# Optimization experiments

Measured on AMD Instinct MI355X. Metric: run time of the kernel, lower is better.

Reference implementation:

```python
import jax, jax.numpy as jnp
import numpy as np

B, L, W, M, NL = 8, 2048, 32, 16, 4  # batch, seq len, width, modes, num_layers


def setup_inputs() -> dict:
    key = jax.random.key(0)
    ks = jax.random.split(key, 16)
    u = lambda k, s: jax.random.uniform(k, s, dtype=jnp.float32)
    n = lambda k, s, sc=0.05: jax.random.normal(k, s, dtype=jnp.float32) * sc
    return {
        "x": jax.random.normal(ks[0], (B, L, 1), dtype=jnp.float32),
        "t": jnp.linspace(0.0, 1.0, L, dtype=jnp.float32),  # grid_x_train
        "fc0_w": n(ks[1], (W, 2), 0.5), "fc0_b": n(ks[2], (W,), 0.1),
        # PR params (torch.rand cfloat -> uniform[0,1) real & imag)
        "pole_re": u(ks[3], (NL, W, W, M)), "pole_im": u(ks[4], (NL, W, W, M)),
        "res_re": u(ks[5], (NL, W, W, M)), "res_im": u(ks[6], (NL, W, W, M)),
        # SpectralConv1d params
        "spec_re": u(ks[7], (NL, W, W, M)), "spec_im": u(ks[8], (NL, W, W, M)),
        # 1x1 Conv1d params
        "conv_w": n(ks[9], (NL, W, W)), "conv_b": n(ks[10], (NL, W), 0.01),
        "fc1_w": n(ks[11], (128, W)), "fc1_b": n(ks[12], (128,), 0.01),
        "fc2_w": n(ks[13], (1, 128)), "fc2_b": n(ks[14], (1,), 0.01),
    }


def reference(x, t, fc0_w, fc0_b, pole_re, pole_im, res_re, res_im,
              spec_re, spec_im, conv_w, conv_b, fc1_w, fc1_b, fc2_w, fc2_b):
    Bx, Lx, _ = x.shape
    gelu = lambda v: jax.nn.gelu(v, approximate=False)
    # get_grid + fc0 + gelu, then (B, L, W) -> (B, W, L)
    grid = jnp.broadcast_to(jnp.linspace(0.0, 1.0, Lx, dtype=x.dtype)[None, :, None], (Bx, Lx, 1))
    h = gelu(jnp.concatenate([x, grid], axis=-1) @ fc0_w.T + fc0_b)
    h = jnp.transpose(h, (0, 2, 1))  # (B, W, L)

    dt = t[1] - t[0]
    # lambda = fftfreq(L, dt) * 2*pi*1j (purely imaginary)
    freqs = jnp.fft.fftfreq(Lx).astype(x.dtype) / dt * (2.0 * np.pi)  # (L,)
    lam = jax.lax.complex(jnp.zeros_like(freqs), freqs)  # complex64 (L,)

    for i in range(NL):
        # --- PR (pole-residue Laplace) branch ---
        pole = jax.lax.complex(pole_re[i], pole_im[i])  # (in, out, M)
        res = jax.lax.complex(res_re[i], res_im[i])     # (in, out, M)
        alpha = jnp.fft.fft(h, axis=-1)  # (B, in, L) complex
        # broadcast-reduce: (in, out, L, M) -> sum over modes -> (in, out, L)
        Hw = (res[:, :, None, :] / (lam[None, None, :, None] - pole[:, :, None, :])).sum(-1)
        pr = jnp.real(jnp.fft.ifft(jnp.einsum('bix,iox->box', alpha, Hw), n=Lx, axis=-1))
        # --- SpectralConv1d branch ---
        spec_w = jax.lax.complex(spec_re[i], spec_im[i])  # (in, out, M)
        xf = jnp.fft.rfft(h, axis=-1)  # (B, in, L//2+1)
        out_ft = jnp.zeros_like(xf).at[:, :, :M].set(
            jnp.einsum('bix,iox->box', xf[:, :, :M], spec_w))
        sc = jnp.fft.irfft(out_ft, n=Lx, axis=-1)
        # --- 1x1 conv branch ---
        wv = jnp.einsum('bil,oi->bol', h, conv_w[i]) + conv_b[i][None, :, None]
        h = gelu(pr + sc + wv)

    h = jnp.transpose(h, (0, 2, 1))  # (B, L, W)
    h = gelu(h @ fc1_w.T + fc1_b)
    return h @ fc2_w.T + fc2_b  # (B, L, 1)
```

## Files before the change

### kernel.cpp

```cpp
#include <hip/hip_runtime.h>
#include <math.h>

#define NFFT   2048
#define M2     1024
#define LOG2N  11
#define BB     8
#define WW     32
#define MM     16
#define NLAYER 4
#define AST    1032

#define PAD(i) ((i) + ((i) >> 5))
#define PADDED_M (M2 + (M2 >> 5))

__device__ __forceinline__ float gelu_f(float v) {
    float ax = fabsf(v) * 0.70710678118654752440f;
    float t  = __builtin_amdgcn_rcpf(fmaf(0.3275911f, ax, 1.0f));
    float s  = fmaf(1.061405429f, t, -1.453152027f);
    s = fmaf(s, t, 1.421413741f);
    s = fmaf(s, t, -0.284496736f);
    s = fmaf(s, t, 0.254829592f);
    s = s * t;
    float e  = __expf(-ax * ax);
    float er = fmaf(-s, e, 1.0f);
    er = copysignf(er, v);
    return 0.5f * v * (1.0f + er);
}

__device__ __forceinline__ float2 cadd(float2 a, float2 b) { return make_float2(a.x + b.x, a.y + b.y); }
__device__ __forceinline__ float2 csub(float2 a, float2 b) { return make_float2(a.x - b.x, a.y - b.y); }
__device__ __forceinline__ float2 cmul(float2 a, float2 b) {
    return make_float2(fmaf(a.x, b.x, -a.y * b.y), fmaf(a.x, b.y, a.y * b.x));
}
template<int S> __device__ __forceinline__ float2 caddi(float2 a, float2 b) {
    return (S > 0) ? make_float2(a.x - b.y, a.y + b.x) : make_float2(a.x + b.y, a.y - b.x);
}
template<int S> __device__ __forceinline__ float2 csubi(float2 a, float2 b) {
    return (S > 0) ? make_float2(a.x + b.y, a.y - b.x) : make_float2(a.x - b.y, a.y + b.x);
}

template<int S> __device__ __forceinline__ void dft4(float2* a) {
    float2 t0 = cadd(a[0], a[2]), t1 = csub(a[0], a[2]);
    float2 t2 = cadd(a[1], a[3]), t3 = csub(a[1], a[3]);
    a[0] = cadd(t0, t2);
    a[2] = csub(t0, t2);
    a[1] = caddi<S>(t1, t3);
    a[3] = csubi<S>(t1, t3);
}

template<int LS, int S>
__device__ __forceinline__ void pass_r4(const float* sre, const float* sim,
                                        float* dre, float* dim, int t) {
    const int s = t & (LS - 1);
    const int q = t / LS;
    float2 a[4];
    #pragma unroll
    for (int r = 0; r < 4; ++r) {
        int idx = t + r * 256;
        a[r] = make_float2(sre[PAD(idx)], sim[PAD(idx)]);
    }
    if (LS > 1) {
        float ph = (6.2831853071795864769f / (4.0f * (float)LS)) * (float)s;
        float sn, cs;
        __sincosf(ph, &sn, &cs);
        float2 w1 = make_float2(cs, (S > 0) ? sn : -sn);
        float2 w2 = cmul(w1, w1);
        a[1] = cmul(a[1], w1);
        a[2] = cmul(a[2], w2);
        a[3] = cmul(a[3], cmul(w2, w1));
    }
    dft4<S>(a);
    int base = q * (4 * LS) + s;
    #pragma unroll
    for (int r = 0; r < 4; ++r) {
        int idx = base + r * LS;
        dre[PAD(idx)] = a[r].x;
        dim[PAD(idx)] = a[r].y;
    }
}

template<int S>
__device__ __forceinline__ void fft1024_g(float* Ar, float* Ai, float* Br, float* Bi,
                                          int t, bool act) {
    if (act) pass_r4<1,   S>(Ar, Ai, Br, Bi, t);
    __syncthreads();
    if (act) pass_r4<4,   S>(Br, Bi, Ar, Ai, t);
    __syncthreads();
    if (act) pass_r4<16,  S>(Ar, Ai, Br, Bi, t);
    __syncthreads();
    if (act) pass_r4<64,  S>(Br, Bi, Ar, Ai, t);
    __syncthreads();
    if (act) pass_r4<256, S>(Ar, Ai, Br, Bi, t);
    __syncthreads();
}

__global__ __launch_bounds__(256) void k_genG_fc0(
    const float* __restrict__ pole_re, const float* __restrict__ pole_im,
    const float* __restrict__ res_re,  const float* __restrict__ res_im,
    const float* __restrict__ spec_re, const float* __restrict__ spec_im,
    const float* __restrict__ conv_w,  const float* __restrict__ tgrid,
    const float* __restrict__ x,       const float* __restrict__ fc0_w,
    const float* __restrict__ fc0_b,
    float2* __restrict__ G, float2* __restrict__ alpha)
{
    __shared__ float Ar[PADDED_M], Ai[PADDED_M], Br[PADDED_M], Bi[PADDED_M];
    int t = threadIdx.x;
    int blk = blockIdx.x;
    float dt = tgrid[1] - tgrid[0];
    float fscale = 6.2831853071795864769f / ((float)NFFT * dt);

    if (blk < NLAYER * WW * WW) {
        int l = blk >> 10, r = blk & 1023, o = r >> 5, i = r & 31;
        int pb = ((l * WW + i) * WW + o) * MM;
        float cw = conv_w[(l * WW + o) * WW + i];
        float wv[4], w2[4];
        float2 acc[4];
        #pragma unroll
        for (int kk = 0; kk < 4; ++kk) {
            wv[kk] = fscale * (float)(t + kk * 256);
            w2[kk] = wv[kk] * wv[kk];
            acc[kk] = make_float2(cw, 0.0f);
        }
        #pragma unroll
        for (int mq = 0; mq < 4; ++mq) {
            float4 P_re = *(const float4*)&pole_re[pb + 4 * mq];
            float4 P_im = *(const float4*)&pole_im[pb + 4 * mq];
            float4 R_re = *(const float4*)&res_re [pb + 4 * mq];
            float4 R_im = *(const float4*)&res_im [pb + 4 * mq];
            #pragma unroll
            for (int mm = 0; mm < 4; ++mm) {
                float Rp = (&P_re.x)[mm], Ip = (&P_im.x)[mm];
                float Rr = (&R_re.x)[mm], Ir = (&R_im.x)[mm];
                float b   = fmaf(Rr, Rp, Ir * Ip);
                float c   = fmaf(Rp, Rp, Ip * Ip);
                float dd  = 2.0f * Rp;
                float dd2 = dd * dd;
                float add = Rr * dd;
                float bdd = b * dd;
                #pragma unroll
                for (int kk = 0; kk < 4; ++kk) {
                    float u   = c - w2[kk];
                    float inv = __builtin_amdgcn_rcpf(fmaf(dd2, w2[kk], u * u));
                    acc[kk].x = fmaf(fmaf(add, w2[kk], b * u), -inv, acc[kk].x);
                    acc[kk].y = fmaf(fmaf(Rr, u, -bdd) * inv, wv[kk], acc[kk].y);
                }
            }
        }
        if (t < MM) {
            if (t) {
                acc[0].x += spec_re[pb + t];
                acc[0].y += spec_im[pb + t];
            } else {
                acc[0].x += spec_re[pb];
            }
        }
        float2* grow = G + (size_t)((l * WW + o) * WW + i) * AST;
        #pragma unroll
        for (int kk = 0; kk < 4; ++kk) grow[t + kk * 256] = acc[kk];
        if (t < 64) {
            float wn = -fscale * (float)M2;
            float accn = cw;
            #pragma unroll
            for (int mq = 0; mq < 4; ++mq) {
                float4 P_re = *(const float4*)&pole_re[pb + 4 * mq];
                float4 P_im = *(const float4*)&pole_im[pb + 4 * mq];
                float4 R_re = *(const float4*)&res_re [pb + 4 * mq];
                float4 R_im = *(const float4*)&res_im [pb + 4 * mq];
                #pragma unroll
                for (int mm = 0; mm < 4; ++mm) {
                    float Rp = (&P_re.x)[mm], Ip = (&P_im.x)[mm];
                    float Rr = (&R_re.x)[mm], Ir = (&R_im.x)[mm];
                    float e   = wn - Ip;
                    float num = fmaf(Ir, e, -(Rr * Rp));
                    float den = fmaf(e, e, Rp * Rp);
                    accn += num * __builtin_amdgcn_rcpf(den);
                }
            }
            if (t == 0) grow[M2] = make_float2(accn, 0.0f);
        }
    } else {
        int row = blk - NLAYER * WW * WW;
        int b = row >> 5, w = row & 31;
        float w0 = fc0_w[2 * w], w1 = fc0_w[2 * w + 1], b0 = fc0_b[w];
        #pragma unroll
        for (int j = 0; j < 8; ++j) {
            int idx = t + j * 256;
            float xv = x[b * NFFT + idx];
            float gv = (float)idx * (1.0f / 2047.0f);
            float val = gelu_f(fmaf(w0, xv, fmaf(w1, gv, b0)));
            int n = idx >> 1;
            if (idx & 1) Ai[PAD(n)] = val;
            else         Ar[PAD(n)] = val;
        }
        __syncthreads();
        fft1024_g<-1>(Ar, Ai, Br, Bi, t, true);
        #pragma unroll
        for (int j = 0; j < 4; ++j) {
            int k  = t + j * 256;
            int mk = (M2 - k) & (M2 - 1);
            float2 Zk  = make_float2(Br[PAD(k)],  Bi[PAD(k)]);
            float2 Zmk = make_float2(Br[PAD(mk)], Bi[PAD(mk)]);
            float2 A  = make_float2(0.5f * (Zk.x + Zmk.x), 0.5f * (Zk.y - Zmk.y));
            float2 Bv = make_float2(0.5f * (Zk.y + Zmk.y), -0.5f * (Zk.x - Zmk.x));
            float ph = (3.1415926535897932385f / (float)M2) * (float)k;
            float sn, cs;
            __sincosf(ph, &sn, &cs);
            float2 e = make_float2(cs, -sn);
            float2 X = cadd(A, cmul(Bv, e));
            float2* arow = alpha + (size_t)row * AST;
            arow[k] = X;
            if (k == 0) arow[M2] = make_float2(A.x - Bv.x, 0.0f);
        }
    }
}

__device__ __forceinline__ void unpack_store512(const float* Br, const float* Bi,
                                                float2* __restrict__ arow, int t) {
    #pragma unroll
    for (int j = 0; j < 2; ++j) {
        int k  = t + j * 512;
        int mk = (M2 - k) & (M2 - 1);
        float2 Zk  = make_float2(Br[PAD(k)],  Bi[PAD(k)]);
        float2 Zmk = make_float2(Br[PAD(mk)], Bi[PAD(mk)]);
        float2 A  = make_float2(0.5f * (Zk.x + Zmk.x), 0.5f * (Zk.y - Zmk.y));
        float2 Bv = make_float2(0.5f * (Zk.y + Zmk.y), -0.5f * (Zk.x - Zmk.x));
        float ph = (3.1415926535897932385f / (float)M2) * (float)k;
        float sn, cs;
        __sincosf(ph, &sn, &cs);
        float2 e = make_float2(cs, -sn);
        float2 X = cadd(A, cmul(Bv, e));
        arow[k] = X;
        if (k == 0)
            arow[M2] = make_float2(A.x - Bv.x, 0.0f);
    }
}

template<bool LAST>
__global__ __launch_bounds__(512) void k_apply_fft(
    const float2* __restrict__ alpha, const float2* __restrict__ G,
    const float* __restrict__ conv_b, float2* __restrict__ alpha_next,
    float2* __restrict__ hout, int layer)
{
    __shared__ float Yr[M2 + 2], Yi[M2 + 2];
    __shared__ float Ar[PADDED_M], Ai[PADDED_M], Br[PADDED_M], Bi[PADDED_M];
    int t = threadIdx.x;
    int row = blockIdx.x;
    int b = row >> 5, o = row & 31;
    const float2* abase = alpha + (size_t)(b * WW) * AST;
    const float2* gbase = G + (size_t)((layer * WW + o) * WW) * AST;

    float2 acc0 = make_float2(0.0f, 0.0f);
    float2 acc1 = make_float2(0.0f, 0.0f);
    #pragma unroll 4
    for (int i = 0; i < 32; ++i) {
        float2 a0 = abase[(size_t)i * AST + t];
        float2 g0 = gbase[(size_t)i * AST + t];
        float2 a1 = abase[(size_t)i * AST + t + 512];
        float2 g1 = gbase[(size_t)i * AST + t + 512];
        acc0.x = fmaf(a0.x, g0.x, fmaf(-a0.y, g0.y, acc0.x));
        acc0.y = fmaf(a0.x, g0.y, fmaf( a0.y, g0.x, acc0.y));
        acc1.x = fmaf(a1.x, g1.x, fmaf(-a1.y, g1.y, acc1.x));
        acc1.y = fmaf(a1.x, g1.y, fmaf( a1.y, g1.x, acc1.y));
    }
    if (t < 64) {
        float p = 0.0f;
        if (t < 32)
            p = abase[(size_t)t * AST + M2].x * gbase[(size_t)t * AST + M2].x;
        #pragma unroll
        for (int off = 16; off >= 1; off >>= 1) p += __shfl_xor(p, off);
        if (t == 0) { Yr[M2] = p; Yi[M2] = 0.0f; }
    }
    if (t == 0) acc0.x += (float)NFFT * conv_b[layer * WW + o];
    Yr[t] = acc0.x;        Yi[t] = acc0.y;
    Yr[t + 512] = acc1.x;  Yi[t + 512] = acc1.y;
    __syncthreads();

    #pragma unroll
    for (int j = 0; j < 2; ++j) {
        int k = t + j * 512;
        float2 Xk = make_float2(Yr[k], Yi[k]);
        float2 Xm = make_float2(Yr[M2 - k], Yi[M2 - k]);
        float2 A = make_float2(0.5f * (Xk.x + Xm.x), 0.5f * (Xk.y - Xm.y));
        float2 u = make_float2(Xk.x - Xm.x, Xk.y + Xm.y);
        float ph = (3.1415926535897932385f / (float)M2) * (float)k;
        float sn, cs;
        __sincosf(ph, &sn, &cs);
        float2 e = make_float2(cs, sn);
        float2 Bv = cmul(u, e);
        Ar[PAD(k)] = A.x - 0.5f * Bv.y;
        Ai[PAD(k)] = A.y + 0.5f * Bv.x;
    }
    __syncthreads();
    fft1024_g<1>(Ar, Ai, Br, Bi, t, t < 256);
    const float invM = 1.0f / (float)M2;
    if (LAST) {
        #pragma unroll
        for (int j = 0; j < 2; ++j) {
            int n = t + j * 512;
            float ge = gelu_f(Br[PAD(n)] * invM);
            float go = gelu_f(Bi[PAD(n)] * invM);
            hout[(size_t)row * M2 + n] = make_float2(ge, go);
        }
    } else {
        #pragma unroll
        for (int j = 0; j < 2; ++j) {
            int n = t + j * 512;
            float ge = gelu_f(Br[PAD(n)] * invM);
            float go = gelu_f(Bi[PAD(n)] * invM);
            Ar[PAD(n)] = ge;
            Ai[PAD(n)] = go;
        }
        __syncthreads();
        fft1024_g<-1>(Ar, Ai, Br, Bi, t, t < 256);
        unpack_store512(Br, Bi, alpha_next + (size_t)row * AST, t);
    }
}

__global__ __launch_bounds__(256) void k_head(
    const float* __restrict__ h, const float* __restrict__ fc1_w,
    const float* __restrict__ fc1_b, const float* __restrict__ fc2_w,
    const float* __restrict__ fc2_b, float* __restrict__ out)
{
    __shared__ float s_w1[128 * 32];
    __shared__ float s_b1[128];
    __shared__ float s_w2[128];
    __shared__ float s_part[4][64];
    int t = threadIdx.x;
    for (int j = t; j < 128 * 32; j += 256) s_w1[j] = fc1_w[j];
    if (t < 128) { s_b1[t] = fc1_b[t]; s_w2[t] = fc2_w[t]; }
    __syncthreads();
    int wv  = t >> 6;
    int ln  = t & 63;
    int pos = blockIdx.x * 64 + ln;
    int b = pos >> LOG2N, l = pos & (NFFT - 1);
    float hreg[32];
    #pragma unroll
    for (int w = 0; w < 32; ++w) hreg[w] = h[(b * WW + w) * NFFT + l];
    float acc = 0.0f;
    int n0 = wv * 32;
    for (int n = n0; n < n0 + 32; ++n) {
        float a = s_b1[n];
        #pragma unroll
        for (int w = 0; w < 32; w += 4) {
            float4 ww = *(const float4*)&s_w1[n * 32 + w];
            a = fmaf(ww.x, hreg[w],     a);
            a = fmaf(ww.y, hreg[w + 1], a);
            a = fmaf(ww.z, hreg[w + 2], a);
            a = fmaf(ww.w, hreg[w + 3], a);
        }
        acc = fmaf(s_w2[n], gelu_f(a), acc);
    }
    s_part[wv][ln] = acc;
    __syncthreads();
    if (t < 64) {
        float r = s_part[0][t] + s_part[1][t] + s_part[2][t] + s_part[3][t] + fc2_b[0];
        out[blockIdx.x * 64 + t] = r;
    }
}

extern "C" void kernel_launch(void* const* d_in, const int* in_sizes, int n_in,
                              void* d_out, int out_size, void* d_ws, size_t ws_size,
                              hipStream_t stream)
{
    const float* x       = (const float*)d_in[0];
    const float* tg      = (const float*)d_in[1];
    const float* fc0_w   = (const float*)d_in[2];
    const float* fc0_b   = (const float*)d_in[3];
    const float* pole_re = (const float*)d_in[4];
    const float* pole_im = (const float*)d_in[5];
    const float* res_re  = (const float*)d_in[6];
    const float* res_im  = (const float*)d_in[7];
    const float* spec_re = (const float*)d_in[8];
    const float* spec_im = (const float*)d_in[9];
    const float* conv_w  = (const float*)d_in[10];
    const float* conv_b  = (const float*)d_in[11];
    const float* fc1_w   = (const float*)d_in[12];
    const float* fc1_b   = (const float*)d_in[13];
    const float* fc2_w   = (const float*)d_in[14];
    const float* fc2_b   = (const float*)d_in[15];
    float* out = (float*)d_out;

    char* ws = (char*)d_ws;
    const size_t plane = (size_t)(BB * WW) * AST * sizeof(float2);
    float2* alphaA = (float2*)ws;
    float2* alphaB = (float2*)(ws + plane);
    float2* hbuf   = (float2*)(ws + 2 * plane);
    float2* Gbuf   = (float2*)(ws + 3 * plane + (size_t)(BB * WW) * M2 * sizeof(float2));

    hipLaunchKernelGGL(k_genG_fc0, dim3(NLAYER * WW * WW + BB * WW), dim3(256), 0, stream,
                       pole_re, pole_im, res_re, res_im, spec_re, spec_im,
                       conv_w, tg, x, fc0_w, fc0_b, Gbuf, alphaA);
    float2* acur = alphaA;
    float2* anxt = alphaB;
    for (int layer = 0; layer < NLAYER; ++layer) {
        if (layer < NLAYER - 1)
            hipLaunchKernelGGL((k_apply_fft<false>), dim3(BB * WW), dim3(512), 0, stream,
                               acur, Gbuf, conv_b, anxt, (float2*)nullptr, layer);
        else
            hipLaunchKernelGGL((k_apply_fft<true>), dim3(BB * WW), dim3(512), 0, stream,
                               acur, Gbuf, conv_b, (float2*)nullptr, hbuf, layer);
        float2* tmp = acur; acur = anxt; anxt = tmp;
    }
    hipLaunchKernelGGL(k_head, dim3(BB * NFFT / 64), dim3(256), 0, stream,
                       (const float*)hbuf, fc1_w, fc1_b, fc2_w, fc2_b, out);
}
```

Baseline: 103.9 us.

## Interleave FFT shared buffers, precompute twiddles, and remap G generation to wavefronts

FFT scratch moves from split real/imag float arrays to interleaved float2 arrays, and each thread computes its per-stage twiddles once with make_tw instead of calling sincos in every radix-4 pass. G generation now assigns one 64-lane wavefront per (layer,o,i) row with 16 frequencies per lane, so four rows share a block and the grid shrinks, and the multiply by wv is hoisted out of the mode loop. The alpha·G contraction loads float4 pairs of adjacent frequencies, and the fc0 input is read as float2. The cost is more registers in the G kernel (16 complex accumulators per lane), which may lower occupancy.

```diff
diff --git a/kernel.cpp b/kernel.cpp
--- a/kernel.cpp
+++ b/kernel.cpp
@@ -49,48 +49,48 @@
 }
 
 template<int LS, int S>
-__device__ __forceinline__ void pass_r4(const float* sre, const float* sim,
-                                        float* dre, float* dim, int t) {
-    const int s = t & (LS - 1);
-    const int q = t / LS;
+__device__ __forceinline__ void pass_cx(const float2* src, float2* dst, int t, float2 w1f) {
     float2 a[4];
     #pragma unroll
-    for (int r = 0; r < 4; ++r) {
-        int idx = t + r * 256;
-        a[r] = make_float2(sre[PAD(idx)], sim[PAD(idx)]);
-    }
+    for (int r = 0; r < 4; ++r) a[r] = src[PAD(t + r * 256)];
     if (LS > 1) {
-        float ph = (6.2831853071795864769f / (4.0f * (float)LS)) * (float)s;
-        float sn, cs;
-        __sincosf(ph, &sn, &cs);
-        float2 w1 = make_float2(cs, (S > 0) ? sn : -sn);
+        float2 w1 = (S > 0) ? make_float2(w1f.x, -w1f.y) : w1f;
         float2 w2 = cmul(w1, w1);
+        float2 w3 = cmul(w2, w1);
         a[1] = cmul(a[1], w1);
         a[2] = cmul(a[2], w2);
-        a[3] = cmul(a[3], cmul(w2, w1));
+        a[3] = cmul(a[3], w3);
     }
     dft4<S>(a);
-    int base = q * (4 * LS) + s;
+    int s = t & (LS - 1);
+    int base = (t / LS) * (4 * LS) + s;
     #pragma unroll
-    for (int r = 0; r < 4; ++r) {
-        int idx = base + r * LS;
-        dre[PAD(idx)] = a[r].x;
-        dim[PAD(idx)] = a[r].y;
-    }
+    for (int r = 0; r < 4; ++r) dst[PAD(base + r * LS)] = a[r];
+}
+
+struct Tw { float2 t4, t16, t64, t256; };
+__device__ __forceinline__ Tw make_tw(int t) {
+    Tw w;
+    float sn, cs;
+    const float c0 = 6.2831853071795864769f;
+    __sincosf(c0 * (float)(t & 3)   * (1.0f / 16.0f),   &sn, &cs); w.t4   = make_float2(cs, -sn);
+    __sincosf(c0 * (float)(t & 15)  * (1.0f / 64.0f),   &sn, &cs); w.t16  = make_float2(cs, -sn);
+    __sincosf(c0 * (float)(t & 63)  * (1.0f / 256.0f),  &sn, &cs); w.t64  = make_float2(cs, -sn);
+    __sincosf(c0 * (float)(t & 255) * (1.0f / 1024.0f), &sn, &cs); w.t256 = make_float2(cs, -sn);
+    return w;
 }
 
 template<int S>
-__device__ __forceinline__ void fft1024_g(float* Ar, float* Ai, float* Br, float* Bi,
-                                          int t, bool act) {
-    if (act) pass_r4<1,   S>(Ar, Ai, Br, Bi, t);
-    __syncthreads();
-    if (act) pass_r4<4,   S>(Br, Bi, Ar, Ai, t);
-    __syncthreads();
-    if (act) pass_r4<16,  S>(Ar, Ai, Br, Bi, t);
-    __syncthreads();
-    if (act) pass_r4<64,  S>(Br, Bi, Ar, Ai, t);
-    __syncthreads();
-    if (act) pass_r4<256, S>(Ar, Ai, Br, Bi, t);
+__device__ __forceinline__ void fft1024_cx(float2* A, float2* B, int t, bool act, const Tw& w) {
+    if (act) pass_cx<1,   S>(A, B, t, make_float2(1.0f, 0.0f));
+    __syncthreads();
+    if (act) pass_cx<4,   S>(B, A, t, w.t4);
+    __syncthreads();
+    if (act) pass_cx<16,  S>(A, B, t, w.t16);
+    __syncthreads();
+    if (act) pass_cx<64,  S>(B, A, t, w.t64);
+    __syncthreads();
+    if (act) pass_cx<256, S>(A, B, t, w.t256);
     __syncthreads();
 }
 
@@ -103,23 +103,25 @@
     const float* __restrict__ fc0_b,
     float2* __restrict__ G, float2* __restrict__ alpha)
 {
-    __shared__ float Ar[PADDED_M], Ai[PADDED_M], Br[PADDED_M], Bi[PADDED_M];
+    __shared__ float2 Acx[PADDED_M], Bcx[PADDED_M];
     int t = threadIdx.x;
     int blk = blockIdx.x;
     float dt = tgrid[1] - tgrid[0];
     float fscale = 6.2831853071795864769f / ((float)NFFT * dt);
 
-    if (blk < NLAYER * WW * WW) {
-        int l = blk >> 10, r = blk & 1023, o = r >> 5, i = r & 31;
+    if (blk < NLAYER * WW * WW / 4) {
+        int lane = t & 63;
+        int u = blk * 4 + (t >> 6);
+        int l = u >> 10, r = u & 1023, o = r >> 5, i = r & 31;
         int pb = ((l * WW + i) * WW + o) * MM;
         float cw = conv_w[(l * WW + o) * WW + i];
-        float wv[4], w2[4];
-        float2 acc[4];
-        #pragma unroll
-        for (int kk = 0; kk < 4; ++kk) {
-            wv[kk] = fscale * (float)(t + kk * 256);
-            w2[kk] = wv[kk] * wv[kk];
-            acc[kk] = make_float2(cw, 0.0f);
+        float w2r[16];
+        float2 acc[16];
+        #pragma unroll
+        for (int j = 0; j < 16; ++j) {
+            float wv = fscale * (float)(lane + 64 * j);
+            w2r[j] = wv * wv;
+            acc[j] = make_float2(cw, 0.0f);
         }
         #pragma unroll
         for (int mq = 0; mq < 4; ++mq) {
@@ -138,26 +140,29 @@
                 float add = Rr * dd;
                 float bdd = b * dd;
                 #pragma unroll
-                for (int kk = 0; kk < 4; ++kk) {
-                    float u   = c - w2[kk];
-                    float inv = __builtin_amdgcn_rcpf(fmaf(dd2, w2[kk], u * u));
-                    acc[kk].x = fmaf(fmaf(add, w2[kk], b * u), -inv, acc[kk].x);
-                    acc[kk].y = fmaf(fmaf(Rr, u, -bdd) * inv, wv[kk], acc[kk].y);
+                for (int j = 0; j < 16; ++j) {
+                    float uu  = c - w2r[j];
+                    float inv = __builtin_amdgcn_rcpf(fmaf(dd2, w2r[j], uu * uu));
+                    acc[j].x = fmaf(fmaf(add, w2r[j], b * uu), -inv, acc[j].x);
+                    acc[j].y = fmaf(fmaf(Rr, uu, -bdd), inv, acc[j].y);
                 }
             }
         }
-        if (t < MM) {
-            if (t) {
-                acc[0].x += spec_re[pb + t];
-                acc[0].y += spec_im[pb + t];
+        #pragma unroll
+        for (int j = 0; j < 16; ++j)
+            acc[j].y *= fscale * (float)(lane + 64 * j);
+        if (lane < MM) {
+            if (lane) {
+                acc[0].x += spec_re[pb + lane];
+                acc[0].y += spec_im[pb + lane];
             } else {
                 acc[0].x += spec_re[pb];
             }
         }
         float2* grow = G + (size_t)((l * WW + o) * WW + i) * AST;
         #pragma unroll
-        for (int kk = 0; kk < 4; ++kk) grow[t + kk * 256] = acc[kk];
-        if (t < 64) {
+        for (int j = 0; j < 16; ++j) grow[lane + 64 * j] = acc[j];
+        if (lane == 0) {
             float wn = -fscale * (float)M2;
             float accn = cw;
             #pragma unroll
@@ -176,30 +181,33 @@
                     accn += num * __builtin_amdgcn_rcpf(den);
                 }
             }
-            if (t == 0) grow[M2] = make_float2(accn, 0.0f);
+            grow[M2] = make_float2(accn, 0.0f);
         }
     } else {
-        int row = blk - NLAYER * WW * WW;
+        int row = blk - NLAYER * WW * WW / 4;
         int b = row >> 5, w = row & 31;
         float w0 = fc0_w[2 * w], w1 = fc0_w[2 * w + 1], b0 = fc0_b[w];
-        #pragma unroll
-        for (int j = 0; j < 8; ++j) {
-            int idx = t + j * 256;
-            float xv = x[b * NFFT + idx];
-            float gv = (float)idx * (1.0f / 2047.0f);
-            float val = gelu_f(fmaf(w0, xv, fmaf(w1, gv, b0)));
-            int n = idx >> 1;
-            if (idx & 1) Ai[PAD(n)] = val;
-            else         Ar[PAD(n)] = val;
+        Tw tw = make_tw(t);
+        const float2* x2 = (const float2*)(x + (size_t)b * NFFT);
+        #pragma unroll
+        for (int j = 0; j < 4; ++j) {
+            int n = t + j * 256;
+            float2 xv = x2[n];
+            float g0 = (float)(2 * n)     * (1.0f / 2047.0f);
+            float g1 = (float)(2 * n + 1) * (1.0f / 2047.0f);
+            float v0 = gelu_f(fmaf(w0, xv.x, fmaf(w1, g0, b0)));
+            float v1 = gelu_f(fmaf(w0, xv.y, fmaf(w1, g1, b0)));
+            Acx[PAD(n)] = make_float2(v0, v1);
         }
         __syncthreads();
-        fft1024_g<-1>(Ar, Ai, Br, Bi, t, true);
+        fft1024_cx<-1>(Acx, Bcx, t, true, tw);
+        float2* arow = alpha + (size_t)row * AST;
         #pragma unroll
         for (int j = 0; j < 4; ++j) {
             int k  = t + j * 256;
             int mk = (M2 - k) & (M2 - 1);
-            float2 Zk  = make_float2(Br[PAD(k)],  Bi[PAD(k)]);
-            float2 Zmk = make_float2(Br[PAD(mk)], Bi[PAD(mk)]);
+            float2 Zk  = Bcx[PAD(k)];
+            float2 Zmk = Bcx[PAD(mk)];
             float2 A  = make_float2(0.5f * (Zk.x + Zmk.x), 0.5f * (Zk.y - Zmk.y));
             float2 Bv = make_float2(0.5f * (Zk.y + Zmk.y), -0.5f * (Zk.x - Zmk.x));
             float ph = (3.1415926535897932385f / (float)M2) * (float)k;
@@ -207,31 +215,9 @@
             __sincosf(ph, &sn, &cs);
             float2 e = make_float2(cs, -sn);
             float2 X = cadd(A, cmul(Bv, e));
-            float2* arow = alpha + (size_t)row * AST;
             arow[k] = X;
             if (k == 0) arow[M2] = make_float2(A.x - Bv.x, 0.0f);
         }
-    }
-}
-
-__device__ __forceinline__ void unpack_store512(const float* Br, const float* Bi,
-                                                float2* __restrict__ arow, int t) {
-    #pragma unroll
-    for (int j = 0; j < 2; ++j) {
-        int k  = t + j * 512;
-        int mk = (M2 - k) & (M2 - 1);
-        float2 Zk  = make_float2(Br[PAD(k)],  Bi[PAD(k)]);
-        float2 Zmk = make_float2(Br[PAD(mk)], Bi[PAD(mk)]);
-        float2 A  = make_float2(0.5f * (Zk.x + Zmk.x), 0.5f * (Zk.y - Zmk.y));
-        float2 Bv = make_float2(0.5f * (Zk.y + Zmk.y), -0.5f * (Zk.x - Zmk.x));
-        float ph = (3.1415926535897932385f / (float)M2) * (float)k;
-        float sn, cs;
-        __sincosf(ph, &sn, &cs);
-        float2 e = make_float2(cs, -sn);
-        float2 X = cadd(A, cmul(Bv, e));
-        arow[k] = X;
-        if (k == 0)
-            arow[M2] = make_float2(A.x - Bv.x, 0.0f);
     }
 }
 
@@ -241,26 +227,28 @@
     const float* __restrict__ conv_b, float2* __restrict__ alpha_next,
     float2* __restrict__ hout, int layer)
 {
-    __shared__ float Yr[M2 + 2], Yi[M2 + 2];
-    __shared__ float Ar[PADDED_M], Ai[PADDED_M], Br[PADDED_M], Bi[PADDED_M];
+    __shared__ __align__(16) float2 Ycx[M2 + 2];
+    __shared__ float2 Acx[PADDED_M], Bcx[PADDED_M];
     int t = threadIdx.x;
     int row = blockIdx.x;
     int b = row >> 5, o = row & 31;
     const float2* abase = alpha + (size_t)(b * WW) * AST;
     const float2* gbase = G + (size_t)((layer * WW + o) * WW) * AST;
+    Tw tw;
+    if (t < 256) tw = make_tw(t);
 
     float2 acc0 = make_float2(0.0f, 0.0f);
     float2 acc1 = make_float2(0.0f, 0.0f);
     #pragma unroll 4
     for (int i = 0; i < 32; ++i) {
-        float2 a0 = abase[(size_t)i * AST + t];
-        float2 g0 = gbase[(size_t)i * AST + t];
-        float2 a1 = abase[(size_t)i * AST + t + 512];
-        float2 g1 = gbase[(size_t)i * AST + t + 512];
-        acc0.x = fmaf(a0.x, g0.x, fmaf(-a0.y, g0.y, acc0.x));
-        acc0.y = fmaf(a0.x, g0.y, fmaf( a0.y, g0.x, acc0.y));
-        acc1.x = fmaf(a1.x, g1.x, fmaf(-a1.y, g1.y, acc1.x));
-        acc1.y = fmaf(a1.x, g1.y, fmaf( a1.y, g1.x, acc1.y));
+        const float4* ar = (const float4*)(abase + (size_t)i * AST);
+        const float4* gr = (const float4*)(gbase + (size_t)i * AST);
+        float4 av = ar[t];
+        float4 gv = gr[t];
+        acc0.x = fmaf(av.x, gv.x, fmaf(-av.y, gv.y, acc0.x));
+        acc0.y = fmaf(av.x, gv.y, fmaf( av.y, gv.x, acc0.y));
+        acc1.x = fmaf(av.z, gv.z, fmaf(-av.w, gv.w, acc1.x));
+        acc1.y = fmaf(av.z, gv.w, fmaf( av.w, gv.z, acc1.y));
     }
     if (t < 64) {
         float p = 0.0f;
@@ -268,18 +256,17 @@
             p = abase[(size_t)t * AST + M2].x * gbase[(size_t)t * AST + M2].x;
         #pragma unroll
         for (int off = 16; off >= 1; off >>= 1) p += __shfl_xor(p, off);
-        if (t == 0) { Yr[M2] = p; Yi[M2] = 0.0f; }
+        if (t == 0) Ycx[M2] = make_float2(p, 0.0f);
     }
     if (t == 0) acc0.x += (float)NFFT * conv_b[layer * WW + o];
-    Yr[t] = acc0.x;        Yi[t] = acc0.y;
-    Yr[t + 512] = acc1.x;  Yi[t + 512] = acc1.y;
+    ((float4*)Ycx)[t] = make_float4(acc0.x, acc0.y, acc1.x, acc1.y);
     __syncthreads();
 
     #pragma unroll
     for (int j = 0; j < 2; ++j) {
         int k = t + j * 512;
-        float2 Xk = make_float2(Yr[k], Yi[k]);
-        float2 Xm = make_float2(Yr[M2 - k], Yi[M2 - k]);
+        float2 Xk = Ycx[k];
+        float2 Xm = Ycx[M2 - k];
         float2 A = make_float2(0.5f * (Xk.x + Xm.x), 0.5f * (Xk.y - Xm.y));
         float2 u = make_float2(Xk.x - Xm.x, Xk.y + Xm.y);
         float ph = (3.1415926535897932385f / (float)M2) * (float)k;
@@ -287,32 +274,44 @@
         __sincosf(ph, &sn, &cs);
         float2 e = make_float2(cs, sn);
         float2 Bv = cmul(u, e);
-        Ar[PAD(k)] = A.x - 0.5f * Bv.y;
-        Ai[PAD(k)] = A.y + 0.5f * Bv.x;
-    }
-    __syncthreads();
-    fft1024_g<1>(Ar, Ai, Br, Bi, t, t < 256);
+        Acx[PAD(k)] = make_float2(A.x - 0.5f * Bv.y, A.y + 0.5f * Bv.x);
+    }
+    __syncthreads();
+    fft1024_cx<1>(Acx, Bcx, t, t < 256, tw);
     const float invM = 1.0f / (float)M2;
     if (LAST) {
         #pragma unroll
         for (int j = 0; j < 2; ++j) {
             int n = t + j * 512;
-            float ge = gelu_f(Br[PAD(n)] * invM);
-            float go = gelu_f(Bi[PAD(n)] * invM);
-            hout[(size_t)row * M2 + n] = make_float2(ge, go);
+            float2 z = Bcx[PAD(n)];
+            hout[(size_t)row * M2 + n] = make_float2(gelu_f(z.x * invM), gelu_f(z.y * invM));
         }
     } else {
         #pragma unroll
         for (int j = 0; j < 2; ++j) {
             int n = t + j * 512;
-            float ge = gelu_f(Br[PAD(n)] * invM);
-            float go = gelu_f(Bi[PAD(n)] * invM);
-            Ar[PAD(n)] = ge;
-            Ai[PAD(n)] = go;
+            float2 z = Bcx[PAD(n)];
+            Acx[PAD(n)] = make_float2(gelu_f(z.x * invM), gelu_f(z.y * invM));
         }
         __syncthreads();
-        fft1024_g<-1>(Ar, Ai, Br, Bi, t, t < 256);
-        unpack_store512(Br, Bi, alpha_next + (size_t)row * AST, t);
+        fft1024_cx<-1>(Acx, Bcx, t, t < 256, tw);
+        float2* arow = alpha_next + (size_t)row * AST;
+        #pragma unroll
+        for (int j = 0; j < 2; ++j) {
+            int k  = t + j * 512;
+            int mk = (M2 - k) & (M2 - 1);
+            float2 Zk  = Bcx[PAD(k)];
+            float2 Zmk = Bcx[PAD(mk)];
+            float2 A  = make_float2(0.5f * (Zk.x + Zmk.x), 0.5f * (Zk.y - Zmk.y));
+            float2 Bv = make_float2(0.5f * (Zk.y + Zmk.y), -0.5f * (Zk.x - Zmk.x));
+            float ph = (3.1415926535897932385f / (float)M2) * (float)k;
+            float sn, cs;
+            __sincosf(ph, &sn, &cs);
+            float2 e = make_float2(cs, -sn);
+            float2 X = cadd(A, cmul(Bv, e));
+            arow[k] = X;
+            if (k == 0) arow[M2] = make_float2(A.x - Bv.x, 0.0f);
+        }
     }
 }
 
@@ -385,9 +384,9 @@
     float2* alphaA = (float2*)ws;
     float2* alphaB = (float2*)(ws + plane);
     float2* hbuf   = (float2*)(ws + 2 * plane);
-    float2* Gbuf   = (float2*)(ws + 3 * plane + (size_t)(BB * WW) * M2 * sizeof(float2));
-
-    hipLaunchKernelGGL(k_genG_fc0, dim3(NLAYER * WW * WW + BB * WW), dim3(256), 0, stream,
+    float2* Gbuf   = (float2*)(ws + 3 * plane);
+
+    hipLaunchKernelGGL(k_genG_fc0, dim3(NLAYER * WW * WW / 4 + BB * WW), dim3(256), 0, stream,
                        pole_re, pole_im, res_re, res_im, spec_re, spec_im,
                        conv_w, tg, x, fc0_w, fc0_b, Gbuf, alphaA);
     float2* acur = alphaA;
```

Result: faster. 90.96 us, median of 3 (-12.4%).
